# Performance work log

Hardware: AMD Instinct MI355X
Metric: run time of the kernel (lower is better)

Reference implementation:

```python
import jax, jax.numpy as jnp
import numpy as np

B, T, D = 2, 2048, 2048
N, K, H = 16, 8, 128            # heads, kv heads, head_dim
SOFT_CAP = 50.0
WINDOW = 1024
SCALE = H ** -0.5               # query_pre_attn_scalar
ROPE_BASE = 10000.0
ROPE_SCALE = 1.0
K_MASK = -2.3819763e+38


def rms_norm(x, scale, eps=1e-6):
    var = jnp.mean(jnp.square(x), axis=-1, keepdims=True)
    return x * jax.lax.rsqrt(var + eps) * (1.0 + scale)


def apply_rope(x, positions):
    # x: [B,T,heads,H]; positions: [B,T] int
    head_dim = x.shape[-1]
    fraction = 2.0 * jnp.arange(head_dim // 2, dtype=jnp.float32) / head_dim
    timescale = ROPE_BASE ** fraction                      # [H/2]
    sinusoid = positions[..., None].astype(jnp.float32) / timescale  # [B,T,H/2]
    sinusoid = sinusoid[..., None, :] / ROPE_SCALE          # [B,T,1,H/2]
    sin, cos = jnp.sin(sinusoid), jnp.cos(sinusoid)
    first, second = jnp.split(x, 2, axis=-1)
    return jnp.concatenate([first * cos - second * sin,
                            second * cos + first * sin], axis=-1)


def setup_inputs() -> dict:
    key = jax.random.key(0)
    ks = jax.random.split(key, 6)
    x = jax.random.normal(ks[0], (B, T, D), jnp.float32)
    q_w = jax.random.normal(ks[1], (N, D, H), jnp.float32) * (D ** -0.5)
    kv_w = jax.random.normal(ks[2], (2, K, D, H), jnp.float32) * (D ** -0.5)
    o_w = jax.random.normal(ks[3], (N, H, D), jnp.float32) * ((N * H) ** -0.5)
    qnorm_scale = 0.1 * jax.random.normal(ks[4], (H,), jnp.float32)
    knorm_scale = 0.1 * jax.random.normal(ks[5], (H,), jnp.float32)
    segment_pos = jnp.broadcast_to(jnp.arange(T, dtype=jnp.int32), (B, T))
    attn_mask = jnp.broadcast_to(jnp.tril(jnp.ones((T, T), dtype=bool)), (B, T, T))
    return {"x": x, "q_w": q_w, "kv_w": kv_w, "o_w": o_w,
            "qnorm_scale": qnorm_scale, "knorm_scale": knorm_scale,
            "segment_pos": segment_pos, "attn_mask": attn_mask}


def reference(x, q_w, kv_w, o_w, qnorm_scale, knorm_scale, segment_pos, attn_mask):
    # projections
    q = jnp.einsum('BTD,NDH->BTNH', x, q_w)            # [B,T,N,H]
    k = jnp.einsum('BSD,KDH->BSKH', x, kv_w[0])        # [B,T,K,H]
    v = jnp.einsum('BSD,KDH->BSKH', x, kv_w[1])
    # QK RMSNorm, then RoPE, then query scaling (matches source order)
    q = apply_rope(rms_norm(q, qnorm_scale), segment_pos) * SCALE
    k = apply_rope(rms_norm(k, knorm_scale), segment_pos)
    # GQA: regroup query heads per kv head
    G = N // K
    qg = q.reshape(B, T, K, G, H)
    logits = jnp.einsum('BTKGH,BSKH->BTKGS', qg, k).reshape(B, T, N, T)
    # logit soft cap
    logits = jnp.tanh(logits / SOFT_CAP) * SOFT_CAP
    # sliding window mask combined with causal attn_mask
    pos_q = segment_pos[:, :, None]
    pos_k = segment_pos[:, None, :]
    sliding = (pos_k > pos_q - WINDOW) & (pos_k < pos_q + WINDOW)
    mask = attn_mask & sliding                          # [B,T,S]
    padded = jnp.where(mask[:, :, None, :], logits, K_MASK)
    probs = jax.nn.softmax(padded, axis=-1).astype(k.dtype)
    enc = jnp.einsum('BTKGS,BSKH->BTKGH',
                     probs.reshape(B, T, K, G, T), v).reshape(B, T, N, H)
    return jnp.einsum('BTNH,NHD->BTD', enc, o_w)
```

## Files before the change

kernel.cpp:

```cpp
#include <hip/hip_runtime.h>
#include <stdint.h>

#define BB 2
#define TT 2048
#define DD 2048
#define NHD 16
#define KVH 8
#define HD 128
#define JC 4096
#define WIN 1024
#define SCALE_Q 0.08838834764831845f

typedef __attribute__((ext_vector_type(8))) short bf16x8;
typedef __attribute__((ext_vector_type(8))) unsigned short us8;
typedef __attribute__((ext_vector_type(4))) unsigned short us4;
typedef __attribute__((ext_vector_type(4))) float f32x4;
typedef __attribute__((ext_vector_type(16))) float f32x16;
typedef __attribute__((ext_vector_type(4))) unsigned int u32x4;

#define GAS __attribute__((address_space(1)))
#define LAS __attribute__((address_space(3)))

__device__ __forceinline__ unsigned short f2bf(float f) {
  unsigned u = __float_as_uint(f);
  u += 0x7FFFu + ((u >> 16) & 1u);
  return (unsigned short)(u >> 16);
}

__device__ __forceinline__ void gload16(const void* g, void* l) {
  __builtin_amdgcn_global_load_lds((const GAS unsigned int*)g, (LAS unsigned int*)l, 16, 0, 0);
}

__global__ void __launch_bounds__(256) k_cvt(const float4* __restrict__ in,
                                             us4* __restrict__ out, int n4) {
  int i = blockIdx.x * 256 + threadIdx.x;
  if (i >= n4) return;
  float4 v = in[i];
  us4 o;
  o[0] = f2bf(v.x); o[1] = f2bf(v.y); o[2] = f2bf(v.z); o[3] = f2bf(v.w);
  out[i] = o;
}

__global__ void __launch_bounds__(256) k_transpose_cvt(
    const float* __restrict__ in, unsigned short* __restrict__ out,
    int R, int C, int ldin, long b0s, int nbi, long b1s, long obs) {
  __shared__ float tile[32][33];
  int z = blockIdx.z;
  const float* ib = in + (long)(z / nbi) * b0s + (long)(z % nbi) * b1s;
  unsigned short* ob = out + (long)z * obs;
  int c0 = blockIdx.x * 32, r0 = blockIdx.y * 32;
  int tx = threadIdx.x, ty = threadIdx.y;
#pragma unroll
  for (int i = 0; i < 4; i++)
    tile[ty + i * 8][tx] = ib[(long)(r0 + ty + i * 8) * ldin + c0 + tx];
  __syncthreads();
#pragma unroll
  for (int i = 0; i < 4; i++)
    ob[(long)(c0 + ty + i * 8) * R + r0 + tx] = f2bf(tile[tx][ty + i * 8]);
}

template <int BM, int BN>
__global__ void __launch_bounds__(512, 2) k_gemm9(
    const unsigned short* __restrict__ A, const unsigned short* __restrict__ Bt,
    float* __restrict__ C, int M, int Nn, int nby) {
  constexpr int KD = 2048;
  constexpr int NT = KD / 32;
  constexpr int ROWS = BM + BN;
  constexpr int IA = BM / 128;
  constexpr int IPT = IA + BN / 128;
  constexpr int MT = BM / 32;
  constexpr int MT2 = MT / 2;
  __shared__ short lds[4][ROWS * 32];

  int tid = threadIdx.x, lane = tid & 63, w = tid >> 6;
  int wm = w >> 2, wn = w & 3;
  int id = blockIdx.x;
  int cpx = gridDim.x >> 3;
  id = (id & 7) * cpx + (id >> 3);
  int m0 = (id / nby) * BM, n0 = (id % nby) * BN;

  int srow = tid >> 2;
  int scol = ((tid & 3) ^ ((tid >> 3) & 3)) * 8;
  const unsigned short* gA = A + (long)(m0 + srow) * KD + scol;
  const unsigned short* gB = Bt + (long)(n0 + srow) * KD + scol;

  auto STG = [&](int p, int ko, int j) {
    if (j < IA)
      gload16(gA + (long)j * 128 * KD + ko, &lds[p][(j * 128 + w * 16) * 32]);
    else
      gload16(gB + (long)(j - IA) * 128 * KD + ko, &lds[p][(BM + (j - IA) * 128 + w * 16) * 32]);
  };

  int frag = (lane & 15) * 32 + (((lane >> 4) ^ ((lane >> 1) & 3)) * 8);
  int abase = wm * (BM / 2) * 32 + frag;
  int bbase = (BM + wn * 64) * 32 + frag;

  f32x4 acc[MT][4] = {};
#pragma unroll
  for (int tt = 0; tt < 3; ++tt)
#pragma unroll
    for (int j = 0; j < IPT; ++j) STG(tt, tt * 32, j);
  if constexpr (IPT == 4) asm volatile("s_waitcnt vmcnt(8)" ::: "memory");
  else                    asm volatile("s_waitcnt vmcnt(6)" ::: "memory");
  __builtin_amdgcn_s_barrier();

  for (int t = 0; t < NT; ++t) {
    const short* bufp = lds[t & 3];
    bool st = (t + 3) < NT;
    int ko = (t + 3) * 32;
    int sp = (t + 3) & 3;
    bf16x8 bfr[4], af[MT2];
#pragma unroll
    for (int ni = 0; ni < 4; ++ni)
      bfr[ni] = *(const bf16x8*)&bufp[bbase + ni * 16 * 32];
#pragma unroll
    for (int mi = 0; mi < MT2; ++mi)
      af[mi] = *(const bf16x8*)&bufp[abase + mi * 16 * 32];
    if (st) { STG(sp, ko, 0); STG(sp, ko, 1); }
    __builtin_amdgcn_s_barrier();
    asm volatile("s_waitcnt lgkmcnt(0)" ::: "memory");
    __builtin_amdgcn_sched_barrier(0);
    __builtin_amdgcn_s_setprio(1);
#pragma unroll
    for (int mi = 0; mi < MT2; ++mi)
#pragma unroll
      for (int ni = 0; ni < 4; ++ni)
        acc[mi][ni] = __builtin_amdgcn_mfma_f32_16x16x32_bf16(af[mi], bfr[ni], acc[mi][ni], 0, 0, 0);
    __builtin_amdgcn_s_setprio(0);
    __builtin_amdgcn_s_barrier();
    bf16x8 af2[MT2];
#pragma unroll
    for (int mi = 0; mi < MT2; ++mi)
      af2[mi] = *(const bf16x8*)&bufp[abase + (MT2 + mi) * 16 * 32];
    if (st) {
#pragma unroll
      for (int j = 2; j < IPT; ++j) STG(sp, ko, j);
    }
    if constexpr (IPT == 4) {
      if (t < NT - 3)       asm volatile("s_waitcnt vmcnt(8)" ::: "memory");
      else if (t == NT - 3) asm volatile("s_waitcnt vmcnt(4)" ::: "memory");
      else if (t < NT - 1)  asm volatile("s_waitcnt vmcnt(0)" ::: "memory");
    } else {
      if (t < NT - 3)       asm volatile("s_waitcnt vmcnt(6)" ::: "memory");
      else if (t == NT - 3) asm volatile("s_waitcnt vmcnt(3)" ::: "memory");
      else if (t < NT - 1)  asm volatile("s_waitcnt vmcnt(0)" ::: "memory");
    }
    __builtin_amdgcn_s_barrier();
    asm volatile("s_waitcnt lgkmcnt(0)" ::: "memory");
    __builtin_amdgcn_sched_barrier(0);
    __builtin_amdgcn_s_setprio(1);
#pragma unroll
    for (int mi = 0; mi < MT2; ++mi)
#pragma unroll
      for (int ni = 0; ni < 4; ++ni)
        acc[MT2 + mi][ni] = __builtin_amdgcn_mfma_f32_16x16x32_bf16(af2[mi], bfr[ni], acc[MT2 + mi][ni], 0, 0, 0);
    __builtin_amdgcn_s_setprio(0);
    __builtin_amdgcn_s_barrier();
  }

#pragma unroll
  for (int mi = 0; mi < MT; mi++)
#pragma unroll
    for (int ni = 0; ni < 4; ni++)
#pragma unroll
      for (int r = 0; r < 4; r++) {
        int row = m0 + wm * (BM / 2) + mi * 16 + (lane >> 4) * 4 + r;
        int col = n0 + wn * 64 + ni * 16 + (lane & 15);
        C[(long)row * Nn + col] = acc[mi][ni][r];
      }
}

__global__ void __launch_bounds__(256) k_norm_rope(
    const float* __restrict__ qkv, const float* __restrict__ qns, const float* __restrict__ kns,
    unsigned short* __restrict__ qb, unsigned short* __restrict__ kb) {
  int wid = threadIdx.x >> 6, lane = threadIdx.x & 63;
  long r = (long)blockIdx.x * 4 + wid;
  int b = (int)(r / (TT * 24));
  int rem = (int)(r % (TT * 24));
  int t = rem / 24, hd = rem % 24;
  const float* row = qkv + (long)(b * TT + t) * JC + (hd < 16 ? hd * HD : 2048 + (hd - 16) * HD);
  float f0 = row[lane], f1 = row[lane + 64];
  float ss = f0 * f0 + f1 * f1;
#pragma unroll
  for (int m = 1; m < 64; m <<= 1) ss += __shfl_xor(ss, m, 64);
  float rinv = rsqrtf(ss * (1.0f / 128.0f) + 1e-6f);
  const float* sc = (hd < 16) ? qns : kns;
  float y0 = f0 * rinv * (1.0f + sc[lane]);
  float y1 = f1 * rinv * (1.0f + sc[lane + 64]);
  float ts = exp2f((float)lane * (13.287712379549449f / 64.0f));
  float ang = (float)t / ts;
  float s, c;
  sincosf(ang, &s, &c);
  float o0 = y0 * c - y1 * s;
  float o1 = y1 * c + y0 * s;
  unsigned short* dst;
  if (hd < 16) {
    o0 *= SCALE_Q; o1 *= SCALE_Q;
    dst = qb + ((long)(b * NHD + hd) * TT + t) * HD;
  } else {
    dst = kb + ((long)(b * KVH + (hd - 16)) * TT + t) * HD;
  }
  dst[lane] = f2bf(o0);
  dst[lane + 64] = f2bf(o1);
}

template <bool FULL>
__device__ __forceinline__ void softcap16(const f32x16& s16, float* pr, float& lsum,
                                          int s_base, int tq, int g) {
#pragma unroll
  for (int r = 0; r < 16; r++) {
    float x = s16[r];
    float e = __builtin_amdgcn_exp2f(-0.05770780163555853f * fabsf(x));
    float u = (x > 0.0f ? e : 1.0f) * __builtin_amdgcn_rcpf(1.0f + e);
    float p = __builtin_amdgcn_exp2f(-144.26950408889634f * u);
    if (!FULL) {
      int s = s_base + (r & 3) + 8 * (r >> 2) + 4 * g;
      bool valid = (s <= tq) && (s > tq - WIN);
      p = valid ? p : 0.0f;
    }
    lsum += p;
    pr[r] = p;
  }
}

__device__ __forceinline__ void hswap(unsigned& a, unsigned& b, int g) {
  unsigned ax = (unsigned)__shfl_xor((int)a, 32, 64);
  unsigned bx = (unsigned)__shfl_xor((int)b, 32, 64);
  unsigned r0 = g ? bx : a;
  unsigned r1 = g ? b : ax;
  a = r0; b = r1;
}

__global__ void __launch_bounds__(256, 2) k_attn(
    const unsigned short* __restrict__ qb, const unsigned short* __restrict__ kb,
    const unsigned short* __restrict__ vbT, unsigned short* __restrict__ enc) {
  __shared__ short Kl[2][64][128];
  __shared__ short Vt[2][128][64];
  int tid = threadIdx.x, lane = tid & 63, w = tid >> 6;
  int g = lane >> 5, l31 = lane & 31;
  int id = blockIdx.x;
  int b = id >> 8;
  int rem = id & 255;
  int n = rem >> 4;
  int traw = rem & 15;
  int tile = b ? ((traw + 8) & 15) : traw;
  int t0 = tile * 128;
  int kh = n >> 1;
  const unsigned short* qbase = qb + ((long)(b * NHD + n) * TT + t0 + w * 32) * HD;
  const unsigned short* kbase = kb + (long)(b * KVH + kh) * TT * HD;
  const unsigned short* vbase = vbT + (long)(b * KVH + kh) * HD * TT;

  bf16x8 bq[8];
  {
    const unsigned short* qp = qbase + (long)l31 * HD + g * 8;
#pragma unroll
    for (int kb8 = 0; kb8 < 8; kb8++)
      bq[kb8] = *(const bf16x8*)(qp + kb8 * 16);
  }

  f32x16 acc[4] = {};
  float lsum = 0.0f;
  int t0w = t0 + w * 32;
  int tq = t0w + l31;
  int s_begin = (t0 >= WIN) ? t0 - WIN : 0;
  int s_end = t0 + 128;

  auto STAGE = [&](int buf, int s0) {
#pragma unroll
    for (int i = 0; i < 4; i++) {
      int row = w * 16 + i * 4 + (lane >> 4);
      int c16 = (lane & 15) ^ (row & 7);
      gload16(kbase + (long)(s0 + row) * HD + c16 * 8, &Kl[buf][w * 16 + i * 4][0]);
    }
#pragma unroll
    for (int i = 0; i < 4; i++) {
      int row = w * 32 + i * 8 + (lane >> 3);
      int c16 = (lane & 7) ^ (row & 7);
      gload16(vbase + (long)row * TT + s0 + c16 * 8, &Vt[buf][w * 32 + i * 8][0]);
    }
  };

  STAGE(0, s_begin);
  __syncthreads();
  int cur = 0;
  for (int s0 = s_begin; s0 < s_end; s0 += 64) {
    if (s0 + 64 < s_end) STAGE(cur ^ 1, s0 + 64);
    bool live = (s0 <= t0w + 31) && (s0 + 63 >= t0w - (WIN - 1));
    if (live) {
      f32x16 sc2[2] = {};
#pragma unroll
      for (int sb = 0; sb < 2; sb++) {
        int srow = sb * 32 + l31;
#pragma unroll
        for (int kb8 = 0; kb8 < 8; kb8++) {
          bf16x8 ak = *(const bf16x8*)&Kl[cur][srow][8 * ((2 * kb8 + g) ^ (srow & 7))];
          sc2[sb] = __builtin_amdgcn_mfma_f32_32x32x16_bf16(ak, bq[kb8], sc2[sb], 0, 0, 0);
        }
      }
      bool full = (s0 + 63 <= t0w) && (s0 >= t0w + 31 - (WIN - 1));
      unsigned pw[4][4];
#pragma unroll
      for (int sb = 0; sb < 2; sb++) {
        float pr[16];
        if (full) softcap16<true>(sc2[sb], pr, lsum, 0, tq, g);
        else      softcap16<false>(sc2[sb], pr, lsum, s0 + sb * 32, tq, g);
        unsigned X[4], Y[4];
#pragma unroll
        for (int m = 0; m < 4; m++) {
          asm("v_cvt_pk_bf16_f32 %0, %1, %2" : "=v"(X[m]) : "v"(pr[4 * m]), "v"(pr[4 * m + 1]));
          asm("v_cvt_pk_bf16_f32 %0, %1, %2" : "=v"(Y[m]) : "v"(pr[4 * m + 2]), "v"(pr[4 * m + 3]));
        }
#pragma unroll
        for (int kl = 0; kl < 2; kl++) {
          hswap(X[2 * kl], X[2 * kl + 1], g);
          hswap(Y[2 * kl], Y[2 * kl + 1], g);
          pw[sb * 2 + kl][0] = X[2 * kl];
          pw[sb * 2 + kl][1] = Y[2 * kl];
          pw[sb * 2 + kl][2] = X[2 * kl + 1];
          pw[sb * 2 + kl][3] = Y[2 * kl + 1];
        }
      }
#pragma unroll
      for (int ks = 0; ks < 4; ks++) {
        u32x4 t4 = {pw[ks][0], pw[ks][1], pw[ks][2], pw[ks][3]};
        bf16x8 pb = __builtin_bit_cast(bf16x8, t4);
#pragma unroll
        for (int ht = 0; ht < 4; ht++) {
          int hrow = ht * 32 + l31;
          bf16x8 av = *(const bf16x8*)&Vt[cur][hrow][8 * ((2 * ks + g) ^ (hrow & 7))];
          acc[ht] = __builtin_amdgcn_mfma_f32_32x32x16_bf16(av, pb, acc[ht], 0, 0, 0);
        }
      }
    }
    __syncthreads();
    cur ^= 1;
  }

  lsum += __shfl_xor(lsum, 32, 64);
  float inv = __builtin_amdgcn_rcpf(lsum);
  unsigned short* dst = enc + ((long)(b * TT + tq) * NHD + n) * HD;
#pragma unroll
  for (int ht = 0; ht < 4; ht++)
#pragma unroll
    for (int r4 = 0; r4 < 4; r4++) {
      us4 o;
#pragma unroll
      for (int e = 0; e < 4; e++) o[e] = f2bf(acc[ht][r4 * 4 + e] * inv);
      *(us4*)(dst + ht * 32 + 8 * r4 + 4 * g) = o;
    }
}

extern "C" void kernel_launch(void* const* d_in, const int* in_sizes, int n_in,
                              void* d_out, int out_size, void* d_ws, size_t ws_size,
                              hipStream_t stream) {
  const float* x    = (const float*)d_in[0];
  const float* q_w  = (const float*)d_in[1];
  const float* kv_w = (const float*)d_in[2];
  const float* o_w  = (const float*)d_in[3];
  const float* qns  = (const float*)d_in[4];
  const float* kns  = (const float*)d_in[5];

  if (ws_size < (104ull << 20)) return;
  char* ws = (char*)d_ws;
  float*          qkv  = (float*)(ws + 0);
  unsigned short* enc  = (unsigned short*)(ws + 0);
  unsigned short* x_bf = (unsigned short*)(ws + (64ll << 20));
  unsigned short* qb   = (unsigned short*)(ws + (64ll << 20));
  unsigned short* Wt   = (unsigned short*)(ws + (80ll << 20));
  unsigned short* kb   = (unsigned short*)(ws + (80ll << 20));
  unsigned short* vbT  = (unsigned short*)(ws + (88ll << 20));
  unsigned short* Wt_o = (unsigned short*)(ws + (96ll << 20));

  dim3 tb(32, 8, 1);
  k_cvt<<<8192, 256, 0, stream>>>((const float4*)x, (us4*)x_bf, 2097152);
  k_transpose_cvt<<<dim3(4, 64, 16), tb, 0, stream>>>(q_w, Wt, 2048, 128, 128,
                                                      0, 16, (long)2048 * 128, (long)128 * 2048);
  k_transpose_cvt<<<dim3(4, 64, 8), tb, 0, stream>>>(kv_w, Wt + (long)2048 * 2048, 2048, 128, 128,
                                                     0, 8, (long)2048 * 128, (long)128 * 2048);
  k_transpose_cvt<<<dim3(4, 64, 8), tb, 0, stream>>>(kv_w + (long)8 * 2048 * 128, Wt + (long)3072 * 2048,
                                                     2048, 128, 128, 0, 8, (long)2048 * 128, (long)128 * 2048);
  k_transpose_cvt<<<dim3(64, 64, 1), tb, 0, stream>>>(o_w, Wt_o, 2048, 2048, 2048, 0, 1, 0, 0);
  k_gemm9<256, 256><<<256, 512, 0, stream>>>(x_bf, Wt, qkv, 4096, 4096, 16);
  k_transpose_cvt<<<dim3(4, 64, 16), tb, 0, stream>>>(qkv + 3072, vbT, 2048, 128, 4096,
                                                      (long)2048 * 4096, 8, 128, (long)128 * 2048);
  k_norm_rope<<<24576, 256, 0, stream>>>(qkv, qns, kns, qb, kb);
  k_attn<<<512, 256, 0, stream>>>(qb, kb, vbT, enc);
  k_gemm9<128, 256><<<256, 512, 0, stream>>>(enc, Wt_o, (float*)d_out, 4096, 2048, 8);
}
```

Baseline: 226.8 us.

## Emit bf16 QKV, merge weight transposes, enlarge attention query tiles, retile output GEMM

The QKV GEMM now writes bf16 instead of fp32, which halves the intermediate traffic read by the V transpose and norm/rope kernels. The three Q/K/V weight transpose launches are merged into one kernel. The attention kernel now has each wave process 64 query rows with two accumulator sets, so K/V tiles staged in LDS are reused across twice as many queries, with half as many blocks and occupancy hint 1. The output projection GEMM is retiled to 256x128 with 256 threads and triple buffering. Rounding QKV to bf16 before RMSNorm adds precision loss, and the larger attention tiles raise register pressure and lower parallelism.

Measured after the change: 250.5 us. 10.4% more time.

```diff
diff --git a/kernel.cpp b/kernel.cpp
--- a/kernel.cpp
+++ b/kernel.cpp
@@ -26,10 +26,15 @@
   u += 0x7FFFu + ((u >> 16) & 1u);
   return (unsigned short)(u >> 16);
 }
+__device__ __forceinline__ float bf2f(unsigned short u) {
+  return __uint_as_float(((unsigned)u) << 16);
+}
 
 __device__ __forceinline__ void gload16(const void* g, void* l) {
   __builtin_amdgcn_global_load_lds((const GAS unsigned int*)g, (LAS unsigned int*)l, 16, 0, 0);
 }
+
+#define VMCNT(n) asm volatile("s_waitcnt vmcnt(" #n ")" ::: "memory")
 
 __global__ void __launch_bounds__(256) k_cvt(const float4* __restrict__ in,
                                              us4* __restrict__ out, int n4) {
@@ -59,21 +64,57 @@
     ob[(long)(c0 + ty + i * 8) * R + r0 + tx] = f2bf(tile[tx][ty + i * 8]);
 }
 
-template <int BM, int BN>
-__global__ void __launch_bounds__(512, 2) k_gemm9(
+__global__ void __launch_bounds__(256) k_wt(const float* __restrict__ qw,
+                                            const float* __restrict__ kvw,
+                                            unsigned short* __restrict__ out) {
+  __shared__ float tile[32][33];
+  int z = blockIdx.z;
+  const float* ib = (z < 16) ? qw + (long)z * 2048 * 128 : kvw + (long)(z - 16) * 2048 * 128;
+  unsigned short* ob = out + (long)z * 128 * 2048;
+  int c0 = blockIdx.x * 32, r0 = blockIdx.y * 32;
+  int tx = threadIdx.x, ty = threadIdx.y;
+#pragma unroll
+  for (int i = 0; i < 4; i++)
+    tile[ty + i * 8][tx] = ib[(long)(r0 + ty + i * 8) * 128 + c0 + tx];
+  __syncthreads();
+#pragma unroll
+  for (int i = 0; i < 4; i++)
+    ob[(long)(c0 + ty + i * 8) * 2048 + r0 + tx] = f2bf(tile[tx][ty + i * 8]);
+}
+
+__global__ void __launch_bounds__(256) k_transpose_bf(
+    const unsigned short* __restrict__ in, unsigned short* __restrict__ out,
+    int R, int C, int ldin, long b0s, int nbi, long b1s, long obs) {
+  __shared__ unsigned short tile[32][33];
+  int z = blockIdx.z;
+  const unsigned short* ib = in + (long)(z / nbi) * b0s + (long)(z % nbi) * b1s;
+  unsigned short* ob = out + (long)z * obs;
+  int c0 = blockIdx.x * 32, r0 = blockIdx.y * 32;
+  int tx = threadIdx.x, ty = threadIdx.y;
+#pragma unroll
+  for (int i = 0; i < 4; i++)
+    tile[ty + i * 8][tx] = ib[(long)(r0 + ty + i * 8) * ldin + c0 + tx];
+  __syncthreads();
+#pragma unroll
+  for (int i = 0; i < 4; i++)
+    ob[(long)(c0 + ty + i * 8) * R + r0 + tx] = tile[tx][ty + i * 8];
+}
+
+template <int BM, int BN, int NWN, int THREADS, int NBUF, bool BF16OUT>
+__global__ void __launch_bounds__(THREADS, 2) k_gemm9(
     const unsigned short* __restrict__ A, const unsigned short* __restrict__ Bt,
-    float* __restrict__ C, int M, int Nn, int nby) {
+    void* __restrict__ Cv, int M, int Nn, int nby) {
   constexpr int KD = 2048;
   constexpr int NT = KD / 32;
   constexpr int ROWS = BM + BN;
-  constexpr int IA = BM / 128;
-  constexpr int IPT = IA + BN / 128;
-  constexpr int MT = BM / 32;
-  constexpr int MT2 = MT / 2;
-  __shared__ short lds[4][ROWS * 32];
+  constexpr int RPI = THREADS / 4;
+  constexpr int IA = BM / RPI;
+  constexpr int IPT = ROWS / RPI;
+  constexpr int MT = 8, MT2 = 4;
+  __shared__ short lds[NBUF][ROWS * 32];
 
   int tid = threadIdx.x, lane = tid & 63, w = tid >> 6;
-  int wm = w >> 2, wn = w & 3;
+  int wm = w / NWN, wn = w % NWN;
   int id = blockIdx.x;
   int cpx = gridDim.x >> 3;
   id = (id & 7) * cpx + (id >> 3);
@@ -86,29 +127,30 @@
 
   auto STG = [&](int p, int ko, int j) {
     if (j < IA)
-      gload16(gA + (long)j * 128 * KD + ko, &lds[p][(j * 128 + w * 16) * 32]);
+      gload16(gA + (long)j * RPI * KD + ko, &lds[p][(j * RPI + w * 16) * 32]);
     else
-      gload16(gB + (long)(j - IA) * 128 * KD + ko, &lds[p][(BM + (j - IA) * 128 + w * 16) * 32]);
+      gload16(gB + (long)(j - IA) * RPI * KD + ko,
+              &lds[p][(BM + (j - IA) * RPI + w * 16) * 32]);
   };
 
   int frag = (lane & 15) * 32 + (((lane >> 4) ^ ((lane >> 1) & 3)) * 8);
-  int abase = wm * (BM / 2) * 32 + frag;
+  int abase = wm * 128 * 32 + frag;
   int bbase = (BM + wn * 64) * 32 + frag;
 
   f32x4 acc[MT][4] = {};
 #pragma unroll
-  for (int tt = 0; tt < 3; ++tt)
+  for (int tt = 0; tt < NBUF - 1; ++tt)
 #pragma unroll
     for (int j = 0; j < IPT; ++j) STG(tt, tt * 32, j);
-  if constexpr (IPT == 4) asm volatile("s_waitcnt vmcnt(8)" ::: "memory");
-  else                    asm volatile("s_waitcnt vmcnt(6)" ::: "memory");
+  if constexpr (IPT * (NBUF - 2) == 8) VMCNT(8);
+  else VMCNT(6);
   __builtin_amdgcn_s_barrier();
 
+  int buf = 0, sp = NBUF - 1;
   for (int t = 0; t < NT; ++t) {
-    const short* bufp = lds[t & 3];
-    bool st = (t + 3) < NT;
-    int ko = (t + 3) * 32;
-    int sp = (t + 3) & 3;
+    const short* bufp = lds[buf];
+    bool st = (t + NBUF - 1) < NT;
+    int ko = (t + NBUF - 1) * 32;
     bf16x8 bfr[4], af[MT2];
 #pragma unroll
     for (int ni = 0; ni < 4; ++ni)
@@ -116,7 +158,10 @@
 #pragma unroll
     for (int mi = 0; mi < MT2; ++mi)
       af[mi] = *(const bf16x8*)&bufp[abase + mi * 16 * 32];
-    if (st) { STG(sp, ko, 0); STG(sp, ko, 1); }
+    if (st) {
+#pragma unroll
+      for (int j = 0; j < IPT / 2; ++j) STG(sp, ko, j);
+    }
     __builtin_amdgcn_s_barrier();
     asm volatile("s_waitcnt lgkmcnt(0)" ::: "memory");
     __builtin_amdgcn_sched_barrier(0);
@@ -134,16 +179,18 @@
       af2[mi] = *(const bf16x8*)&bufp[abase + (MT2 + mi) * 16 * 32];
     if (st) {
 #pragma unroll
-      for (int j = 2; j < IPT; ++j) STG(sp, ko, j);
-    }
-    if constexpr (IPT == 4) {
-      if (t < NT - 3)       asm volatile("s_waitcnt vmcnt(8)" ::: "memory");
-      else if (t == NT - 3) asm volatile("s_waitcnt vmcnt(4)" ::: "memory");
-      else if (t < NT - 1)  asm volatile("s_waitcnt vmcnt(0)" ::: "memory");
-    } else {
-      if (t < NT - 3)       asm volatile("s_waitcnt vmcnt(6)" ::: "memory");
-      else if (t == NT - 3) asm volatile("s_waitcnt vmcnt(3)" ::: "memory");
-      else if (t < NT - 1)  asm volatile("s_waitcnt vmcnt(0)" ::: "memory");
+      for (int j = IPT / 2; j < IPT; ++j) STG(sp, ko, j);
+    }
+    {
+      int rem = NT - 2 - t;
+      if (rem > NBUF - 2) rem = NBUF - 2;
+      if (rem == 2) {
+        if constexpr (IPT == 4) VMCNT(8); else VMCNT(12);
+      } else if (rem == 1) {
+        if constexpr (IPT == 4) VMCNT(4); else VMCNT(6);
+      } else if (rem == 0) {
+        VMCNT(0);
+      }
     }
     __builtin_amdgcn_s_barrier();
     asm volatile("s_waitcnt lgkmcnt(0)" ::: "memory");
@@ -156,6 +203,8 @@
         acc[MT2 + mi][ni] = __builtin_amdgcn_mfma_f32_16x16x32_bf16(af2[mi], bfr[ni], acc[MT2 + mi][ni], 0, 0, 0);
     __builtin_amdgcn_s_setprio(0);
     __builtin_amdgcn_s_barrier();
+    buf = (buf == NBUF - 1) ? 0 : buf + 1;
+    sp = (sp == NBUF - 1) ? 0 : sp + 1;
   }
 
 #pragma unroll
@@ -164,22 +213,26 @@
     for (int ni = 0; ni < 4; ni++)
 #pragma unroll
       for (int r = 0; r < 4; r++) {
-        int row = m0 + wm * (BM / 2) + mi * 16 + (lane >> 4) * 4 + r;
+        int row = m0 + wm * 128 + mi * 16 + (lane >> 4) * 4 + r;
         int col = n0 + wn * 64 + ni * 16 + (lane & 15);
-        C[(long)row * Nn + col] = acc[mi][ni][r];
+        if constexpr (BF16OUT)
+          ((unsigned short*)Cv)[(long)row * Nn + col] = f2bf(acc[mi][ni][r]);
+        else
+          ((float*)Cv)[(long)row * Nn + col] = acc[mi][ni][r];
       }
 }
 
 __global__ void __launch_bounds__(256) k_norm_rope(
-    const float* __restrict__ qkv, const float* __restrict__ qns, const float* __restrict__ kns,
+    const unsigned short* __restrict__ qkv, const float* __restrict__ qns,
+    const float* __restrict__ kns,
     unsigned short* __restrict__ qb, unsigned short* __restrict__ kb) {
   int wid = threadIdx.x >> 6, lane = threadIdx.x & 63;
   long r = (long)blockIdx.x * 4 + wid;
   int b = (int)(r / (TT * 24));
   int rem = (int)(r % (TT * 24));
   int t = rem / 24, hd = rem % 24;
-  const float* row = qkv + (long)(b * TT + t) * JC + (hd < 16 ? hd * HD : 2048 + (hd - 16) * HD);
-  float f0 = row[lane], f1 = row[lane + 64];
+  const unsigned short* row = qkv + (long)(b * TT + t) * JC + (hd < 16 ? hd * HD : 2048 + (hd - 16) * HD);
+  float f0 = bf2f(row[lane]), f1 = bf2f(row[lane + 64]);
   float ss = f0 * f0 + f1 * f1;
 #pragma unroll
   for (int m = 1; m < 64; m <<= 1) ss += __shfl_xor(ss, m, 64);
@@ -231,7 +284,7 @@
   a = r0; b = r1;
 }
 
-__global__ void __launch_bounds__(256, 2) k_attn(
+__global__ void __launch_bounds__(256, 1) k_attn(
     const unsigned short* __restrict__ qb, const unsigned short* __restrict__ kb,
     const unsigned short* __restrict__ vbT, unsigned short* __restrict__ enc) {
   __shared__ short Kl[2][64][128];
@@ -239,31 +292,30 @@
   int tid = threadIdx.x, lane = tid & 63, w = tid >> 6;
   int g = lane >> 5, l31 = lane & 31;
   int id = blockIdx.x;
-  int b = id >> 8;
-  int rem = id & 255;
-  int n = rem >> 4;
-  int traw = rem & 15;
-  int tile = b ? ((traw + 8) & 15) : traw;
-  int t0 = tile * 128;
+  int b = id >> 7;
+  int rem = id & 127;
+  int n = rem >> 3;
+  int ti = rem & 7;
+  int t0 = ti * 256;
   int kh = n >> 1;
-  const unsigned short* qbase = qb + ((long)(b * NHD + n) * TT + t0 + w * 32) * HD;
+  const unsigned short* qbase = qb + ((long)(b * NHD + n) * TT + t0 + w * 64) * HD;
   const unsigned short* kbase = kb + (long)(b * KVH + kh) * TT * HD;
   const unsigned short* vbase = vbT + (long)(b * KVH + kh) * HD * TT;
 
-  bf16x8 bq[8];
-  {
-    const unsigned short* qp = qbase + (long)l31 * HD + g * 8;
+  bf16x8 bq[2][8];
+#pragma unroll
+  for (int qg = 0; qg < 2; qg++) {
+    const unsigned short* qp = qbase + (long)(qg * 32 + l31) * HD + g * 8;
 #pragma unroll
     for (int kb8 = 0; kb8 < 8; kb8++)
-      bq[kb8] = *(const bf16x8*)(qp + kb8 * 16);
+      bq[qg][kb8] = *(const bf16x8*)(qp + kb8 * 16);
   }
 
-  f32x16 acc[4] = {};
-  float lsum = 0.0f;
-  int t0w = t0 + w * 32;
-  int tq = t0w + l31;
+  f32x16 acc0[4] = {}, acc1[4] = {};
+  float lsum0 = 0.0f, lsum1 = 0.0f;
+  int t0w = t0 + w * 64;
   int s_begin = (t0 >= WIN) ? t0 - WIN : 0;
-  int s_end = t0 + 128;
+  int s_end = t0 + 256;
 
   auto STAGE = [&](int buf, int s0) {
 #pragma unroll
@@ -277,6 +329,30 @@
       int row = w * 32 + i * 8 + (lane >> 3);
       int c16 = (lane & 7) ^ (row & 7);
       gload16(vbase + (long)row * TT + s0 + c16 * 8, &Vt[buf][w * 32 + i * 8][0]);
+    }
+  };
+
+  auto PROC = [&](const f32x16& sv, int qg, float& ls, unsigned (*pwp)[4], int sb, int s0) {
+    int base = t0w + qg * 32;
+    int tq = base + l31;
+    float pr[16];
+    bool fullg = (s0 + 63 <= base) && (s0 >= base + 32 - WIN);
+    if (fullg) softcap16<true>(sv, pr, ls, 0, tq, g);
+    else       softcap16<false>(sv, pr, ls, s0 + sb * 32, tq, g);
+    unsigned X[4], Y[4];
+#pragma unroll
+    for (int m = 0; m < 4; m++) {
+      asm("v_cvt_pk_bf16_f32 %0, %1, %2" : "=v"(X[m]) : "v"(pr[4 * m]), "v"(pr[4 * m + 1]));
+      asm("v_cvt_pk_bf16_f32 %0, %1, %2" : "=v"(Y[m]) : "v"(pr[4 * m + 2]), "v"(pr[4 * m + 3]));
+    }
+#pragma unroll
+    for (int kl = 0; kl < 2; kl++) {
+      hswap(X[2 * kl], X[2 * kl + 1], g);
+      hswap(Y[2 * kl], Y[2 * kl + 1], g);
+      pwp[sb * 2 + kl][0] = X[2 * kl];
+      pwp[sb * 2 + kl][1] = Y[2 * kl];
+      pwp[sb * 2 + kl][2] = X[2 * kl + 1];
+      pwp[sb * 2 + kl][3] = Y[2 * kl + 1];
     }
   };
 
@@ -285,50 +361,34 @@
   int cur = 0;
   for (int s0 = s_begin; s0 < s_end; s0 += 64) {
     if (s0 + 64 < s_end) STAGE(cur ^ 1, s0 + 64);
-    bool live = (s0 <= t0w + 31) && (s0 + 63 >= t0w - (WIN - 1));
+    bool live = (s0 <= t0w + 63) && (s0 + 63 >= t0w - (WIN - 1));
     if (live) {
-      f32x16 sc2[2] = {};
+      unsigned pw0[4][4], pw1[4][4];
 #pragma unroll
       for (int sb = 0; sb < 2; sb++) {
         int srow = sb * 32 + l31;
+        f32x16 s0v = {}, s1v = {};
 #pragma unroll
         for (int kb8 = 0; kb8 < 8; kb8++) {
           bf16x8 ak = *(const bf16x8*)&Kl[cur][srow][8 * ((2 * kb8 + g) ^ (srow & 7))];
-          sc2[sb] = __builtin_amdgcn_mfma_f32_32x32x16_bf16(ak, bq[kb8], sc2[sb], 0, 0, 0);
+          s0v = __builtin_amdgcn_mfma_f32_32x32x16_bf16(ak, bq[0][kb8], s0v, 0, 0, 0);
+          s1v = __builtin_amdgcn_mfma_f32_32x32x16_bf16(ak, bq[1][kb8], s1v, 0, 0, 0);
         }
+        PROC(s0v, 0, lsum0, pw0, sb, s0);
+        PROC(s1v, 1, lsum1, pw1, sb, s0);
       }
-      bool full = (s0 + 63 <= t0w) && (s0 >= t0w + 31 - (WIN - 1));
-      unsigned pw[4][4];
-#pragma unroll
-      for (int sb = 0; sb < 2; sb++) {
-        float pr[16];
-        if (full) softcap16<true>(sc2[sb], pr, lsum, 0, tq, g);
-        else      softcap16<false>(sc2[sb], pr, lsum, s0 + sb * 32, tq, g);
-        unsigned X[4], Y[4];
-#pragma unroll
-        for (int m = 0; m < 4; m++) {
-          asm("v_cvt_pk_bf16_f32 %0, %1, %2" : "=v"(X[m]) : "v"(pr[4 * m]), "v"(pr[4 * m + 1]));
-          asm("v_cvt_pk_bf16_f32 %0, %1, %2" : "=v"(Y[m]) : "v"(pr[4 * m + 2]), "v"(pr[4 * m + 3]));
-        }
-#pragma unroll
-        for (int kl = 0; kl < 2; kl++) {
-          hswap(X[2 * kl], X[2 * kl + 1], g);
-          hswap(Y[2 * kl], Y[2 * kl + 1], g);
-          pw[sb * 2 + kl][0] = X[2 * kl];
-          pw[sb * 2 + kl][1] = Y[2 * kl];
-          pw[sb * 2 + kl][2] = X[2 * kl + 1];
-          pw[sb * 2 + kl][3] = Y[2 * kl + 1];
-        }
-      }
 #pragma unroll
       for (int ks = 0; ks < 4; ks++) {
-        u32x4 t4 = {pw[ks][0], pw[ks][1], pw[ks][2], pw[ks][3]};
-        bf16x8 pb = __builtin_bit_cast(bf16x8, t4);
+        u32x4 t40 = {pw0[ks][0], pw0[ks][1], pw0[ks][2], pw0[ks][3]};
+        u32x4 t41 = {pw1[ks][0], pw1[ks][1], pw1[ks][2], pw1[ks][3]};
+        bf16x8 pb0 = __builtin_bit_cast(bf16x8, t40);
+        bf16x8 pb1 = __builtin_bit_cast(bf16x8, t41);
 #pragma unroll
         for (int ht = 0; ht < 4; ht++) {
           int hrow = ht * 32 + l31;
           bf16x8 av = *(const bf16x8*)&Vt[cur][hrow][8 * ((2 * ks + g) ^ (hrow & 7))];
-          acc[ht] = __builtin_amdgcn_mfma_f32_32x32x16_bf16(av, pb, acc[ht], 0, 0, 0);
+          acc0[ht] = __builtin_amdgcn_mfma_f32_32x32x16_bf16(av, pb0, acc0[ht], 0, 0, 0);
+          acc1[ht] = __builtin_amdgcn_mfma_f32_32x32x16_bf16(av, pb1, acc1[ht], 0, 0, 0);
         }
       }
     }
@@ -336,17 +396,24 @@
     cur ^= 1;
   }
 
-  lsum += __shfl_xor(lsum, 32, 64);
-  float inv = __builtin_amdgcn_rcpf(lsum);
-  unsigned short* dst = enc + ((long)(b * TT + tq) * NHD + n) * HD;
+  lsum0 += __shfl_xor(lsum0, 32, 64);
+  lsum1 += __shfl_xor(lsum1, 32, 64);
+  float inv0 = __builtin_amdgcn_rcpf(lsum0);
+  float inv1 = __builtin_amdgcn_rcpf(lsum1);
+  unsigned short* dst0 = enc + ((long)(b * TT + t0w + l31) * NHD + n) * HD;
+  unsigned short* dst1 = enc + ((long)(b * TT + t0w + 32 + l31) * NHD + n) * HD;
 #pragma unroll
   for (int ht = 0; ht < 4; ht++)
 #pragma unroll
     for (int r4 = 0; r4 < 4; r4++) {
-      us4 o;
-#pragma unroll
-      for (int e = 0; e < 4; e++) o[e] = f2bf(acc[ht][r4 * 4 + e] * inv);
-      *(us4*)(dst + ht * 32 + 8 * r4 + 4 * g) = o;
+      us4 o0, o1;
+#pragma unroll
+      for (int e = 0; e < 4; e++) {
+        o0[e] = f2bf(acc0[ht][r4 * 4 + e] * inv0);
+        o1[e] = f2bf(acc1[ht][r4 * 4 + e] * inv1);
+      }
+      *(us4*)(dst0 + ht * 32 + 8 * r4 + 4 * g) = o0;
+      *(us4*)(dst1 + ht * 32 + 8 * r4 + 4 * g) = o1;
     }
 }
 
@@ -362,7 +429,7 @@
 
   if (ws_size < (104ull << 20)) return;
   char* ws = (char*)d_ws;
-  float*          qkv  = (float*)(ws + 0);
+  unsigned short* qkvb = (unsigned short*)(ws + 0);
   unsigned short* enc  = (unsigned short*)(ws + 0);
   unsigned short* x_bf = (unsigned short*)(ws + (64ll << 20));
   unsigned short* qb   = (unsigned short*)(ws + (64ll << 20));
@@ -373,17 +440,12 @@
 
   dim3 tb(32, 8, 1);
   k_cvt<<<8192, 256, 0, stream>>>((const float4*)x, (us4*)x_bf, 2097152);
-  k_transpose_cvt<<<dim3(4, 64, 16), tb, 0, stream>>>(q_w, Wt, 2048, 128, 128,
-                                                      0, 16, (long)2048 * 128, (long)128 * 2048);
-  k_transpose_cvt<<<dim3(4, 64, 8), tb, 0, stream>>>(kv_w, Wt + (long)2048 * 2048, 2048, 128, 128,
-                                                     0, 8, (long)2048 * 128, (long)128 * 2048);
-  k_transpose_cvt<<<dim3(4, 64, 8), tb, 0, stream>>>(kv_w + (long)8 * 2048 * 128, Wt + (long)3072 * 2048,
-                                                     2048, 128, 128, 0, 8, (long)2048 * 128, (long)128 * 2048);
+  k_wt<<<dim3(4, 64, 32), tb, 0, stream>>>(q_w, kv_w, Wt);
   k_transpose_cvt<<<dim3(64, 64, 1), tb, 0, stream>>>(o_w, Wt_o, 2048, 2048, 2048, 0, 1, 0, 0);
-  k_gemm9<256, 256><<<256, 512, 0, stream>>>(x_bf, Wt, qkv, 4096, 4096, 16);
-  k_transpose_cvt<<<dim3(4, 64, 16), tb, 0, stream>>>(qkv + 3072, vbT, 2048, 128, 4096,
-                                                      (long)2048 * 4096, 8, 128, (long)128 * 2048);
-  k_norm_rope<<<24576, 256, 0, stream>>>(qkv, qns, kns, qb, kb);
-  k_attn<<<512, 256, 0, stream>>>(qb, kb, vbT, enc);
-  k_gemm9<128, 256><<<256, 512, 0, stream>>>(enc, Wt_o, (float*)d_out, 4096, 2048, 8);
-}
+  k_gemm9<256, 256, 4, 512, 4, true><<<256, 512, 0, stream>>>(x_bf, Wt, qkvb, 4096, 4096, 16);
+  k_transpose_bf<<<dim3(4, 64, 16), tb, 0, stream>>>(qkvb + 3072, vbT, 2048, 128, 4096,
+                                                     (long)2048 * 4096, 8, 128, (long)128 * 2048);
+  k_norm_rope<<<24576, 256, 0, stream>>>(qkvb, qns, kns, qb, kb);
+  k_attn<<<256, 256, 0, stream>>>(qb, kb, vbT, enc);
+  k_gemm9<256, 128, 2, 256, 3, false><<<256, 256, 0, stream>>>(enc, Wt_o, (float*)d_out, 4096, 2048, 16);
+}
```
